# Optimization experiments

Hardware: AMD Instinct MI355X
Metric: run time of the kernel (lower is better)

Reference implementation:

```python
import jax, jax.numpy as jnp
import numpy as np

N = 50000        # n_nodes
E = 1_600_000    # n_edges (avg degree 32)
IN = 128         # in_dim
H = 8            # num_heads
R = 16           # hidden_rank
D = 16           # out_dim (per head)
SCALE = float(np.sqrt(D))


def setup_inputs() -> dict:
    key = jax.random.key(0)
    k1, k2, k3, k4, k5, k6 = jax.random.split(key, 6)
    h = jax.random.normal(k1, (N, IN), jnp.float32)
    src = jax.random.randint(k2, (E,), 0, N, dtype=jnp.int32)
    dst = jax.random.randint(k3, (E,), 0, N, dtype=jnp.int32)
    s = 1.0 / np.sqrt(IN)  # kaiming-ish scale
    p = jax.random.normal(k4, (IN, H * R), jnp.float32) * s
    q = jax.random.normal(k5, (IN, H * R), jnp.float32) * s
    Wv = jax.random.normal(k6, (IN, H * D), jnp.float32) * s
    return {"h": h, "src": src, "dst": dst, "p": p, "q": q, "Wv": Wv}


def reference(h, src, dst, p, q, Wv):
    # global_attention_type == 'transform' -> atted = h
    K = (h @ q).reshape(N, H, R)   # K_h = atted @ _q
    Q = (h @ p).reshape(N, H, R)   # Q_h = h @ _p
    V = (h @ Wv).reshape(N, H, D)  # V_h = V(h), no bias
    # per-edge score: (K[src] * Q[dst]).sum(-1, keepdim), then scaled exp
    score = jnp.sum(K[src] * Q[dst], axis=-1, keepdims=True)   # [E, H, 1]
    score = jnp.exp(jnp.clip(score / SCALE, -5.0, 5.0))
    # scatter-sum into destination nodes
    wV = jax.ops.segment_sum(V[src] * score, dst, num_segments=N)  # [N, H, D]
    z = jax.ops.segment_sum(score, dst, num_segments=N)            # [N, H, 1]
    z = jnp.where(z == 0, jnp.float32(0.001), z)
    return wV / z
```

## Files before the change

### kernel.cpp

```cpp
#include <hip/hip_runtime.h>
#include <hip/hip_fp16.h>


#define HNODE 64
#define EPB   8192
#define BKT_SHIFT 7
#define BKT_CAP 5120

typedef _Float16 f16x8 __attribute__((ext_vector_type(8)));
typedef float    f32x4 __attribute__((ext_vector_type(4)));
typedef _Float16 hv2   __attribute__((ext_vector_type(2)));

__device__ __forceinline__ float fdot2(unsigned a, unsigned b, float c) {
#if __has_builtin(__builtin_amdgcn_fdot2)
    return __builtin_amdgcn_fdot2(__builtin_bit_cast(hv2, a),
                                  __builtin_bit_cast(hv2, b), c, false);
#else
    __half2 ah = *(__half2*)&a, bh = *(__half2*)&b;
    float2 af = __half22float2(ah), bf = __half22float2(bh);
    return c + af.x * bf.x + af.y * bf.y;
#endif
}

__device__ __forceinline__ float2 h2f(unsigned u) {
    __half2 hh = *(__half2*)&u;
    return __half22float2(hh);
}

__device__ __forceinline__ unsigned pack2(float a, float b) {
    __half2 hh = __floats2half2_rn(a, b);
    return *(unsigned*)&hh;
}

__global__ __launch_bounds__(256) void wt_convert_kernel(
    const float* __restrict__ Wq, const float* __restrict__ Wp,
    const float* __restrict__ Wv, __half* __restrict__ Wt)
{
    int o = blockIdx.x * 256 + threadIdx.x;
    int m = o >> 14, rem = o & 16383;
    int nn = rem >> 7, kk = rem & 127;
    const float* W = (m == 0) ? Wq : (m == 1) ? Wp : Wv;
    Wt[o] = __float2half(W[kk * 128 + nn]);
}

__global__ __launch_bounds__(256) void gemm_kqv_kernel(
    const float* __restrict__ h, const __half* __restrict__ Wt,
    unsigned* __restrict__ KV, __half* __restrict__ Q, int n)
{
    __shared__ __align__(16) char smem[34816];
    _Float16* ws = (_Float16*)smem;
    float*    Cs = (float*)smem;

    const int t = threadIdx.x;
    const int wid = t >> 6, lane = t & 63;
    const int node0 = blockIdx.x * HNODE;
    const int mrow = lane & 15, quad = lane >> 4;

    int row = node0 + wid * 16 + mrow;
    if (row >= n) row = n - 1;
    f16x8 afr[4];
    #pragma unroll
    for (int s = 0; s < 4; s++) {
        const float4* hp = (const float4*)(h + (size_t)row * 128 + quad * 8 + 32 * s);
        float4 f0 = hp[0], f1 = hp[1];
        f16x8 a;
        a[0] = (_Float16)f0.x; a[1] = (_Float16)f0.y;
        a[2] = (_Float16)f0.z; a[3] = (_Float16)f0.w;
        a[4] = (_Float16)f1.x; a[5] = (_Float16)f1.y;
        a[6] = (_Float16)f1.z; a[7] = (_Float16)f1.w;
        afr[s] = a;
    }

    const int er = t >> 2;
    const int eq0 = (t & 3) * 8;
    const int egn = node0 + er;
    unsigned kq[16];

    #pragma unroll
    for (int m = 0; m < 3; m++) {
        __syncthreads();
        {
            const uint4* wg = (const uint4*)(Wt + (size_t)m * 16384);
            #pragma unroll
            for (int i = 0; i < 8; i++) {
                int idx = t * 8 + i;
                int r = idx >> 4, seg = idx & 15;
                *(uint4*)(ws + r * 136 + seg * 8) = wg[idx];
            }
        }
        __syncthreads();

        f32x4 acc[8];
        #pragma unroll
        for (int ct = 0; ct < 8; ct++) acc[ct] = (f32x4){0.f, 0.f, 0.f, 0.f};

        #pragma unroll
        for (int s = 0; s < 4; s++) {
            #pragma unroll
            for (int ct = 0; ct < 8; ct++) {
                f16x8 b = *(const f16x8*)(ws + (ct * 16 + mrow) * 136 + quad * 8 + 32 * s);
                acc[ct] = __builtin_amdgcn_mfma_f32_16x16x32_f16(afr[s], b, acc[ct], 0, 0, 0);
            }
        }

        __syncthreads();
        #pragma unroll
        for (int ct = 0; ct < 8; ct++) {
            int col = ct * 16 + mrow;
            int r0 = wid * 16 + quad * 4;
            Cs[(r0 + 0) * 132 + col] = acc[ct][0];
            Cs[(r0 + 1) * 132 + col] = acc[ct][1];
            Cs[(r0 + 2) * 132 + col] = acc[ct][2];
            Cs[(r0 + 3) * 132 + col] = acc[ct][3];
        }
        __syncthreads();

        float c[32];
        {
            const float* src = Cs + er * 132 + eq0 * 4;
            #pragma unroll
            for (int i = 0; i < 8; i++) {
                float4 v = *(const float4*)(src + i * 4);
                c[4 * i + 0] = v.x; c[4 * i + 1] = v.y;
                c[4 * i + 2] = v.z; c[4 * i + 3] = v.w;
            }
        }
        if (m == 0) {
            #pragma unroll
            for (int j = 0; j < 8; j++) {
                kq[2 * j]     = pack2(c[4 * j],     c[4 * j + 1]);
                kq[2 * j + 1] = pack2(c[4 * j + 2], c[4 * j + 3]);
            }
        } else if (m == 1) {
            if (egn < n) {
                uint4* qp = (uint4*)(Q + (size_t)egn * 128) + (t & 3) * 4;
                #pragma unroll
                for (int i = 0; i < 4; i++) {
                    uint4 ov;
                    ov.x = pack2(c[8 * i + 0], c[8 * i + 1]);
                    ov.y = pack2(c[8 * i + 2], c[8 * i + 3]);
                    ov.z = pack2(c[8 * i + 4], c[8 * i + 5]);
                    ov.w = pack2(c[8 * i + 6], c[8 * i + 7]);
                    qp[i] = ov;
                }
            }
        } else {
            if (egn < n) {
                uint4* kvp = (uint4*)(KV + (size_t)egn * 128);
                #pragma unroll
                for (int j = 0; j < 8; j++) {
                    uint4 ov;
                    ov.x = kq[2 * j];
                    ov.y = kq[2 * j + 1];
                    ov.z = pack2(c[4 * j],     c[4 * j + 1]);
                    ov.w = pack2(c[4 * j + 2], c[4 * j + 3]);
                    kvp[eq0 + j] = ov;
                }
            }
        }
    }
}

__global__ __launch_bounds__(256) void bucket_scatter_kernel(
    const int* __restrict__ src, const int* __restrict__ dst,
    int* __restrict__ bucket_cursor, int2* __restrict__ ebuf, int E, int nbkt)
{
    __shared__ int cnt[512];
    __shared__ int start[512];
    int t = threadIdx.x;
    for (int i = t; i < nbkt; i += 256) cnt[i] = 0;
    __syncthreads();

    int4 sv[8], dv[8];
    int base = blockIdx.x * EPB + t * 4;
    #pragma unroll
    for (int r = 0; r < 8; r++) {
        int i = base + r * 1024;
        if (i + 3 < E) {
            sv[r] = *(const int4*)(src + i);
            dv[r] = *(const int4*)(dst + i);
        } else {
            int ts[4], td[4];
            for (int k = 0; k < 4; k++) {
                int j = i + k;
                ts[k] = (j < E) ? src[j] : 0;
                td[k] = (j < E) ? dst[j] : -1;
            }
            sv[r] = make_int4(ts[0], ts[1], ts[2], ts[3]);
            dv[r] = make_int4(td[0], td[1], td[2], td[3]);
        }
        if (dv[r].x >= 0) atomicAdd(&cnt[dv[r].x >> BKT_SHIFT], 1);
        if (dv[r].y >= 0) atomicAdd(&cnt[dv[r].y >> BKT_SHIFT], 1);
        if (dv[r].z >= 0) atomicAdd(&cnt[dv[r].z >> BKT_SHIFT], 1);
        if (dv[r].w >= 0) atomicAdd(&cnt[dv[r].w >> BKT_SHIFT], 1);
    }
    __syncthreads();
    for (int i = t; i < nbkt; i += 256) {
        int c = cnt[i];
        start[i] = c ? atomicAdd(&bucket_cursor[i], c) : 0;
        cnt[i] = 0;
    }
    __syncthreads();
    #pragma unroll
    for (int r = 0; r < 8; r++) {
        int s, d, b, pl;
        d = dv[r].x; if (d >= 0) { s = sv[r].x; b = d >> BKT_SHIFT; pl = start[b] + atomicAdd(&cnt[b], 1); if (pl < BKT_CAP) ebuf[(size_t)b * BKT_CAP + pl] = make_int2(s, d); }
        d = dv[r].y; if (d >= 0) { s = sv[r].y; b = d >> BKT_SHIFT; pl = start[b] + atomicAdd(&cnt[b], 1); if (pl < BKT_CAP) ebuf[(size_t)b * BKT_CAP + pl] = make_int2(s, d); }
        d = dv[r].z; if (d >= 0) { s = sv[r].z; b = d >> BKT_SHIFT; pl = start[b] + atomicAdd(&cnt[b], 1); if (pl < BKT_CAP) ebuf[(size_t)b * BKT_CAP + pl] = make_int2(s, d); }
        d = dv[r].w; if (d >= 0) { s = sv[r].w; b = d >> BKT_SHIFT; pl = start[b] + atomicAdd(&cnt[b], 1); if (pl < BKT_CAP) ebuf[(size_t)b * BKT_CAP + pl] = make_int2(s, d); }
    }
}

__global__ __launch_bounds__(256) void fine_scatter_kernel(
    const int2* __restrict__ ebuf, const int* __restrict__ bucket_cursor,
    int2* __restrict__ offs, int* __restrict__ csr, int N, int nbkt)
{
    __shared__ int ldeg[128];
    __shared__ int lcur[128];
    int b = blockIdx.x, t = threadIdx.x;
    int node_base = b << BKT_SHIFT;
    int seg0 = b * BKT_CAP;
    int cnt = bucket_cursor[b];
    if (cnt > BKT_CAP) cnt = BKT_CAP;

    if (t < 128) ldeg[t] = 0;
    __syncthreads();
    for (int i = t; i < cnt; i += 256)
        atomicAdd(&ldeg[ebuf[seg0 + i].y - node_base], 1);
    __syncthreads();
    int mydeg = (t < 128) ? ldeg[t] : 0;
    for (int off = 1; off < 128; off <<= 1) {
        int y = (t >= off && t < 128) ? ldeg[t - off] : 0;
        __syncthreads();
        if (t < 128) ldeg[t] += y;
        __syncthreads();
    }
    if (t < 128) {
        int incl = ldeg[t];
        int gbeg = seg0 + incl - mydeg;
        lcur[t] = gbeg;
        int node = node_base + t;
        if (node < N) offs[node] = make_int2(gbeg, seg0 + incl);
    }
    __syncthreads();
    for (int i = t; i < cnt; i += 256) {
        int2 ed = ebuf[seg0 + i];
        int pos = atomicAdd(&lcur[ed.y - node_base], 1);
        csr[pos] = ed.x;
    }
}

__global__ __launch_bounds__(256) void aggregate_kernel(
    const uint4* __restrict__ KV, const uint2* __restrict__ Qr,
    const int2* __restrict__ offs, const int* __restrict__ csr,
    float4* __restrict__ out, int n)
{
    int t = threadIdx.x;
    int node = blockIdx.x * 8 + (t >> 5);
    if (node >= n) return;
    int lane = t & 31;

    uint2 qq = Qr[(size_t)node * 32 + lane];
    int2 be = offs[node];
    int beg = be.x, end = be.y;

    float4 accV = make_float4(0.f, 0.f, 0.f, 0.f);
    float accZ = 0.f;

    int chunk = beg;
    int myidx = (chunk + lane < end) ? csr[chunk + lane] : 0;

    uint4 kv0 = make_uint4(0,0,0,0), kv1 = make_uint4(0,0,0,0);
    if (beg < end)     kv0 = KV[(size_t)__shfl(myidx, 0, 32) * 32 + lane];
    if (beg + 1 < end) kv1 = KV[(size_t)__shfl(myidx, 1, 32) * 32 + lane];

    for (int e = beg; e < end; e += 2) {
        int e2 = e + 2;
        uint4 nkv0, nkv1;
        bool m0 = (e2 < end), m1 = (e2 + 1 < end);
        if (m0) {
            int off = e2 - chunk;
            if (off == 32) {
                chunk = e2;
                myidx = (chunk + lane < end) ? csr[chunk + lane] : 0;
                off = 0;
            }
            nkv0 = KV[(size_t)__shfl(myidx, off, 32) * 32 + lane];
            if (m1) nkv1 = KV[(size_t)__shfl(myidx, off + 1, 32) * 32 + lane];
        }
        {
            float p = fdot2(kv0.x, qq.x, fdot2(kv0.y, qq.y, 0.f));
            p += __shfl_xor(p, 1);
            p += __shfl_xor(p, 2);
            float x = fminf(fmaxf(p * 0.25f, -5.f), 5.f);
            float sc = __expf(x);
            accZ += sc;
            float2 va = h2f(kv0.z), vb = h2f(kv0.w);
            accV.x += sc * va.x; accV.y += sc * va.y;
            accV.z += sc * vb.x; accV.w += sc * vb.y;
        }
        if (e + 1 < end) {
            float p = fdot2(kv1.x, qq.x, fdot2(kv1.y, qq.y, 0.f));
            p += __shfl_xor(p, 1);
            p += __shfl_xor(p, 2);
            float x = fminf(fmaxf(p * 0.25f, -5.f), 5.f);
            float sc = __expf(x);
            accZ += sc;
            float2 va = h2f(kv1.z), vb = h2f(kv1.w);
            accV.x += sc * va.x; accV.y += sc * va.y;
            accV.z += sc * vb.x; accV.w += sc * vb.y;
        }
        if (m0) kv0 = nkv0;
        if (m1) kv1 = nkv1;
    }
    if (accZ == 0.f) accZ = 0.001f;
    float inv = 1.0f / accZ;
    out[(size_t)node * 32 + lane] =
        make_float4(accV.x * inv, accV.y * inv, accV.z * inv, accV.w * inv);
}


extern "C" void kernel_launch(void* const* d_in, const int* in_sizes, int n_in,
                              void* d_out, int out_size, void* d_ws, size_t ws_size,
                              hipStream_t stream)
{
    const float* h   = (const float*)d_in[0];
    const int*   src = (const int*)d_in[1];
    const int*   dst = (const int*)d_in[2];
    const float* p   = (const float*)d_in[3];
    const float* q   = (const float*)d_in[4];
    const float* wv  = (const float*)d_in[5];
    float* out = (float*)d_out;

    const int N = in_sizes[0] / 128;
    const int E = in_sizes[1];
    const int nbkt = (N + 127) >> BKT_SHIFT;

    unsigned* KV = (unsigned*)d_ws;
    __half* Qh   = (__half*)(KV + (size_t)N * 128);
    int2* ebuf   = (int2*)(Qh + (size_t)N * 128);
    int* csr     = (int*)(ebuf + (size_t)nbkt * BKT_CAP);
    int2* offs   = (int2*)(csr + (size_t)nbkt * BKT_CAP);
    int* bucket_cursor = (int*)(offs + N);
    __half* Wt   = (__half*)(bucket_cursor + 512);

    (void)hipMemsetAsync(bucket_cursor, 0, 512 * sizeof(int), stream);

    wt_convert_kernel<<<192, 256, 0, stream>>>(q, p, wv, Wt);

    int nblk_e = (E + EPB - 1) / EPB;
    bucket_scatter_kernel<<<nblk_e, 256, 0, stream>>>(src, dst, bucket_cursor, ebuf, E, nbkt);

    gemm_kqv_kernel<<<(N + HNODE - 1) / HNODE, 256, 0, stream>>>(h, Wt, KV, Qh, N);

    fine_scatter_kernel<<<nbkt, 256, 0, stream>>>(ebuf, bucket_cursor, offs, csr, N, nbkt);

    aggregate_kernel<<<(N + 7) / 8, 256, 0, stream>>>(
        (const uint4*)KV, (const uint2*)Qh, offs, csr, (float4*)out, N);
}
```

Measured before the change: 260.5 us.

## Transpose GEMM MFMA for direct stores; process two edges per wave in aggregate

The KQV GEMM swaps the MFMA operands so that each lane holds output rows directly. All three projections are accumulated in registers and written straight to global memory, with no LDS staging round-trip or the extra barriers it needed. The aggregate kernel now gives each node a full 64-lane wave, and the two 32-lane halves process alternating edges. The halves combine their partial sums with a cross-half shuffle at the end. This costs more registers in the GEMM (96 accumulator floats) and halves the nodes per block in aggregate.

```diff
diff --git a/kernel.cpp b/kernel.cpp
--- a/kernel.cpp
+++ b/kernel.cpp
@@ -47,34 +47,35 @@
     const float* __restrict__ h, const __half* __restrict__ Wt,
     unsigned* __restrict__ KV, __half* __restrict__ Q, int n)
 {
-    __shared__ __align__(16) char smem[34816];
-    _Float16* ws = (_Float16*)smem;
-    float*    Cs = (float*)smem;
+    __shared__ __align__(16) _Float16 ws[128 * 136];
 
     const int t = threadIdx.x;
     const int wid = t >> 6, lane = t & 63;
     const int node0 = blockIdx.x * HNODE;
     const int mrow = lane & 15, quad = lane >> 4;
 
-    int row = node0 + wid * 16 + mrow;
-    if (row >= n) row = n - 1;
-    f16x8 afr[4];
+    const int row = node0 + wid * 16 + mrow;
+    const bool rowvalid = (row < n);
+    const int rowc = rowvalid ? row : (n - 1);
+
+    f16x8 hfr[4];
     #pragma unroll
     for (int s = 0; s < 4; s++) {
-        const float4* hp = (const float4*)(h + (size_t)row * 128 + quad * 8 + 32 * s);
+        const float4* hp = (const float4*)(h + (size_t)rowc * 128 + quad * 8 + 32 * s);
         float4 f0 = hp[0], f1 = hp[1];
         f16x8 a;
         a[0] = (_Float16)f0.x; a[1] = (_Float16)f0.y;
         a[2] = (_Float16)f0.z; a[3] = (_Float16)f0.w;
         a[4] = (_Float16)f1.x; a[5] = (_Float16)f1.y;
         a[6] = (_Float16)f1.z; a[7] = (_Float16)f1.w;
-        afr[s] = a;
-    }
-
-    const int er = t >> 2;
-    const int eq0 = (t & 3) * 8;
-    const int egn = node0 + er;
-    unsigned kq[16];
+        hfr[s] = a;
+    }
+
+    f32x4 acc[3][8];
+    #pragma unroll
+    for (int m = 0; m < 3; m++)
+        #pragma unroll
+        for (int ct = 0; ct < 8; ct++) acc[m][ct] = (f32x4){0.f, 0.f, 0.f, 0.f};
 
     #pragma unroll
     for (int m = 0; m < 3; m++) {
@@ -89,74 +90,32 @@
             }
         }
         __syncthreads();
-
-        f32x4 acc[8];
-        #pragma unroll
-        for (int ct = 0; ct < 8; ct++) acc[ct] = (f32x4){0.f, 0.f, 0.f, 0.f};
-
         #pragma unroll
         for (int s = 0; s < 4; s++) {
             #pragma unroll
             for (int ct = 0; ct < 8; ct++) {
-                f16x8 b = *(const f16x8*)(ws + (ct * 16 + mrow) * 136 + quad * 8 + 32 * s);
-                acc[ct] = __builtin_amdgcn_mfma_f32_16x16x32_f16(afr[s], b, acc[ct], 0, 0, 0);
+                f16x8 a = *(const f16x8*)(ws + (ct * 16 + mrow) * 136 + quad * 8 + 32 * s);
+                acc[m][ct] = __builtin_amdgcn_mfma_f32_16x16x32_f16(a, hfr[s], acc[m][ct], 0, 0, 0);
             }
         }
-
-        __syncthreads();
+    }
+
+    if (rowvalid) {
+        unsigned* kvrow = KV + (size_t)row * 128;
+        __half*   qrow  = Q  + (size_t)row * 128;
         #pragma unroll
         for (int ct = 0; ct < 8; ct++) {
-            int col = ct * 16 + mrow;
-            int r0 = wid * 16 + quad * 4;
-            Cs[(r0 + 0) * 132 + col] = acc[ct][0];
-            Cs[(r0 + 1) * 132 + col] = acc[ct][1];
-            Cs[(r0 + 2) * 132 + col] = acc[ct][2];
-            Cs[(r0 + 3) * 132 + col] = acc[ct][3];
-        }
-        __syncthreads();
-
-        float c[32];
-        {
-            const float* src = Cs + er * 132 + eq0 * 4;
-            #pragma unroll
-            for (int i = 0; i < 8; i++) {
-                float4 v = *(const float4*)(src + i * 4);
-                c[4 * i + 0] = v.x; c[4 * i + 1] = v.y;
-                c[4 * i + 2] = v.z; c[4 * i + 3] = v.w;
-            }
-        }
-        if (m == 0) {
-            #pragma unroll
-            for (int j = 0; j < 8; j++) {
-                kq[2 * j]     = pack2(c[4 * j],     c[4 * j + 1]);
-                kq[2 * j + 1] = pack2(c[4 * j + 2], c[4 * j + 3]);
-            }
-        } else if (m == 1) {
-            if (egn < n) {
-                uint4* qp = (uint4*)(Q + (size_t)egn * 128) + (t & 3) * 4;
-                #pragma unroll
-                for (int i = 0; i < 4; i++) {
-                    uint4 ov;
-                    ov.x = pack2(c[8 * i + 0], c[8 * i + 1]);
-                    ov.y = pack2(c[8 * i + 2], c[8 * i + 3]);
-                    ov.z = pack2(c[8 * i + 4], c[8 * i + 5]);
-                    ov.w = pack2(c[8 * i + 6], c[8 * i + 7]);
-                    qp[i] = ov;
-                }
-            }
-        } else {
-            if (egn < n) {
-                uint4* kvp = (uint4*)(KV + (size_t)egn * 128);
-                #pragma unroll
-                for (int j = 0; j < 8; j++) {
-                    uint4 ov;
-                    ov.x = kq[2 * j];
-                    ov.y = kq[2 * j + 1];
-                    ov.z = pack2(c[4 * j],     c[4 * j + 1]);
-                    ov.w = pack2(c[4 * j + 2], c[4 * j + 3]);
-                    kvp[eq0 + j] = ov;
-                }
-            }
+            int qd = ct * 4 + quad;
+            uint4 ov;
+            ov.x = pack2(acc[0][ct][0], acc[0][ct][1]);
+            ov.y = pack2(acc[0][ct][2], acc[0][ct][3]);
+            ov.z = pack2(acc[2][ct][0], acc[2][ct][1]);
+            ov.w = pack2(acc[2][ct][2], acc[2][ct][3]);
+            *(uint4*)(kvrow + 4 * qd) = ov;
+            uint2 qv;
+            qv.x = pack2(acc[1][ct][0], acc[1][ct][1]);
+            qv.y = pack2(acc[1][ct][2], acc[1][ct][3]);
+            *(uint2*)(qrow + 4 * qd) = qv;
         }
     }
 }
@@ -256,67 +215,65 @@
     float4* __restrict__ out, int n)
 {
     int t = threadIdx.x;
-    int node = blockIdx.x * 8 + (t >> 5);
+    int node = blockIdx.x * 4 + (t >> 6);
     if (node >= n) return;
-    int lane = t & 31;
-
-    uint2 qq = Qr[(size_t)node * 32 + lane];
+    int lane = t & 63;
+    int l = lane & 31;
+    int eh = lane >> 5;
+
+    uint2 qq = Qr[(size_t)node * 32 + l];
     int2 be = offs[node];
-    int beg = be.x, end = be.y;
+    int beg = be.x, cnt = be.y - be.x;
 
     float4 accV = make_float4(0.f, 0.f, 0.f, 0.f);
     float accZ = 0.f;
 
-    int chunk = beg;
-    int myidx = (chunk + lane < end) ? csr[chunk + lane] : 0;
-
-    uint4 kv0 = make_uint4(0,0,0,0), kv1 = make_uint4(0,0,0,0);
-    if (beg < end)     kv0 = KV[(size_t)__shfl(myidx, 0, 32) * 32 + lane];
-    if (beg + 1 < end) kv1 = KV[(size_t)__shfl(myidx, 1, 32) * 32 + lane];
-
-    for (int e = beg; e < end; e += 2) {
-        int e2 = e + 2;
-        uint4 nkv0, nkv1;
-        bool m0 = (e2 < end), m1 = (e2 + 1 < end);
-        if (m0) {
-            int off = e2 - chunk;
-            if (off == 32) {
-                chunk = e2;
-                myidx = (chunk + lane < end) ? csr[chunk + lane] : 0;
+    int chunkbase = 0;
+    int myidx = (beg + lane < be.y) ? csr[beg + lane] : 0;
+
+    uint4 kv = make_uint4(0, 0, 0, 0);
+    if (cnt > 0) {
+        int s0 = __shfl(myidx, eh, 64);
+        kv = KV[(size_t)s0 * 32 + l];
+    }
+
+    for (int e = 0; e < cnt; e += 2) {
+        uint4 nkv;
+        bool more = (e + 2 < cnt);
+        if (more) {
+            int off = e + 2 - chunkbase;
+            if (off == 64) {
+                chunkbase = e + 2;
+                myidx = (beg + chunkbase + lane < be.y) ? csr[beg + chunkbase + lane] : 0;
                 off = 0;
             }
-            nkv0 = KV[(size_t)__shfl(myidx, off, 32) * 32 + lane];
-            if (m1) nkv1 = KV[(size_t)__shfl(myidx, off + 1, 32) * 32 + lane];
-        }
-        {
-            float p = fdot2(kv0.x, qq.x, fdot2(kv0.y, qq.y, 0.f));
-            p += __shfl_xor(p, 1);
-            p += __shfl_xor(p, 2);
-            float x = fminf(fmaxf(p * 0.25f, -5.f), 5.f);
-            float sc = __expf(x);
-            accZ += sc;
-            float2 va = h2f(kv0.z), vb = h2f(kv0.w);
-            accV.x += sc * va.x; accV.y += sc * va.y;
-            accV.z += sc * vb.x; accV.w += sc * vb.y;
-        }
-        if (e + 1 < end) {
-            float p = fdot2(kv1.x, qq.x, fdot2(kv1.y, qq.y, 0.f));
-            p += __shfl_xor(p, 1);
-            p += __shfl_xor(p, 2);
-            float x = fminf(fmaxf(p * 0.25f, -5.f), 5.f);
-            float sc = __expf(x);
-            accZ += sc;
-            float2 va = h2f(kv1.z), vb = h2f(kv1.w);
-            accV.x += sc * va.x; accV.y += sc * va.y;
-            accV.z += sc * vb.x; accV.w += sc * vb.y;
-        }
-        if (m0) kv0 = nkv0;
-        if (m1) kv1 = nkv1;
-    }
-    if (accZ == 0.f) accZ = 0.001f;
-    float inv = 1.0f / accZ;
-    out[(size_t)node * 32 + lane] =
-        make_float4(accV.x * inv, accV.y * inv, accV.z * inv, accV.w * inv);
+            int sn = __shfl(myidx, off + eh, 64);
+            nkv = KV[(size_t)sn * 32 + l];
+        }
+        float p = fdot2(kv.x, qq.x, fdot2(kv.y, qq.y, 0.f));
+        p += __shfl_xor(p, 1);
+        p += __shfl_xor(p, 2);
+        float x = fminf(fmaxf(p * 0.25f, -5.f), 5.f);
+        float sc = (e + eh < cnt) ? __expf(x) : 0.f;
+        accZ += sc;
+        float2 va = h2f(kv.z), vb = h2f(kv.w);
+        accV.x += sc * va.x; accV.y += sc * va.y;
+        accV.z += sc * vb.x; accV.w += sc * vb.y;
+        if (more) kv = nkv;
+    }
+
+    accZ  += __shfl_xor(accZ, 32);
+    accV.x += __shfl_xor(accV.x, 32);
+    accV.y += __shfl_xor(accV.y, 32);
+    accV.z += __shfl_xor(accV.z, 32);
+    accV.w += __shfl_xor(accV.w, 32);
+
+    if (lane < 32) {
+        if (accZ == 0.f) accZ = 0.001f;
+        float inv = 1.0f / accZ;
+        out[(size_t)node * 32 + l] =
+            make_float4(accV.x * inv, accV.y * inv, accV.z * inv, accV.w * inv);
+    }
 }
 
 
@@ -355,6 +312,6 @@
 
     fine_scatter_kernel<<<nbkt, 256, 0, stream>>>(ebuf, bucket_cursor, offs, csr, N, nbkt);
 
-    aggregate_kernel<<<(N + 7) / 8, 256, 0, stream>>>(
+    aggregate_kernel<<<(N + 3) / 4, 256, 0, stream>>>(
         (const uint4*)KV, (const uint2*)Qh, offs, csr, (float4*)out, N);
 }
```

Result: faster. 252.8 us (-2.9%).
